# Performance work log

Measured on AMD Instinct MI355X. Metric: run time of the kernel, lower is better.

The kernel has to match this reference:

```python
import jax, jax.numpy as jnp
import numpy as np

N_NODES, N_EDGES, D_FEAT, HIDDEN, N_CLASSES = 100000, 3200000, 128, 16, 40


def setup_inputs() -> dict:
    key = jax.random.key(0)
    ks = jax.random.split(key, 6)
    x = jax.random.normal(ks[0], (N_NODES, D_FEAT), dtype=jnp.float32)
    edge_index = jax.random.randint(ks[1], (2, N_EDGES), 0, N_NODES, dtype=jnp.int32)
    # SAGEConv params: lin_l (aggregated neighbors, with bias), lin_r (root, no bias)
    W_l = jax.random.normal(ks[2], (D_FEAT, HIDDEN), dtype=jnp.float32) / np.sqrt(D_FEAT)
    b_l = jnp.zeros((HIDDEN,), jnp.float32)
    W_r = jax.random.normal(ks[3], (D_FEAT, HIDDEN), dtype=jnp.float32) / np.sqrt(D_FEAT)
    # final Linear(hidden, num_classes)
    W3 = jax.random.normal(ks[4], (HIDDEN, N_CLASSES), dtype=jnp.float32) / np.sqrt(HIDDEN)
    b3 = jnp.zeros((N_CLASSES,), jnp.float32)
    return {"x": x, "edge_index": edge_index, "W_l": W_l, "b_l": b_l,
            "W_r": W_r, "W3": W3, "b3": b3}


def reference(x, edge_index, W_l, b_l, W_r, W3, b3):
    N = x.shape[0]
    src, dst = edge_index[0], edge_index[1]
    # mean aggregation of source features onto target nodes (PyG source_to_target)
    agg = jax.ops.segment_sum(x[src], dst, num_segments=N)            # [N, F]
    deg = jax.ops.segment_sum(jnp.ones_like(dst, dtype=x.dtype), dst, num_segments=N)
    mean = agg / jnp.maximum(deg, 1.0)[:, None]                        # zero-in-degree -> 0
    # SAGEConv: lin_l(mean) + lin_r(x)
    h = mean @ W_l + b_l + x @ W_r                                     # [N, 16]
    h = jax.nn.relu(h)
    logits = h @ W3 + b3                                               # [N, C]
    return jax.nn.log_softmax(logits, axis=1)
```

## Files before the change

kernel.cpp:

```cpp
#include <hip/hip_runtime.h>
#include <hip/hip_bf16.h>

#define D_FEAT 128
#define HIDDEN 16
#define NCLS 40
#define EPB 4096
#define FXSCALE 262144.0f
#define FXINV   (1.0f / 262144.0f)

typedef unsigned int uint;

__device__ __forceinline__ uint f2bf(float x) {
  uint u = __float_as_uint(x);
  return (u + 0x7FFFu + ((u >> 16) & 1u)) >> 16;
}

__global__ __launch_bounds__(256) void lin_kernel(
    const float* __restrict__ x,
    const float* __restrict__ Wl, const float* __restrict__ Wr,
    uint* __restrict__ ylb, float* __restrict__ yr, int N) {
  __shared__ float sW[D_FEAT][8][4];
  __shared__ float sx[32][132];

  int tid = threadIdx.x;
  for (int idx = tid; idx < D_FEAT * 32; idx += 256) {
    int k = idx >> 5, o = idx & 31;
    float v = (o < 16) ? Wl[k * 16 + o] : Wr[k * 16 + (o - 16)];
    sW[k][o >> 2][o & 3] = v;
  }

  int row0 = blockIdx.x * 32;
  for (int q = tid; q < 32 * 32; q += 256) {
    int r = q >> 5, k4 = q & 31;
    int row = row0 + r;
    float4 v = make_float4(0.f, 0.f, 0.f, 0.f);
    if (row < N) v = *(const float4*)(x + (size_t)row * D_FEAT + k4 * 4);
    *(float4*)(&sx[r][k4 * 4]) = v;
  }
  __syncthreads();

  int r = tid >> 3, oq = tid & 7;
  int row = row0 + r;
  if (row < N) {
    float4 acc = make_float4(0.f, 0.f, 0.f, 0.f);
#pragma unroll
    for (int k = 0; k < D_FEAT; ++k) {
      float xv = sx[r][k];
      const float4 w = *(const float4*)(&sW[k][oq][0]);
      acc.x += xv * w.x; acc.y += xv * w.y;
      acc.z += xv * w.z; acc.w += xv * w.w;
    }
    if (oq < 4) {
      uint2 pk;
      pk.x = f2bf(acc.x) | (f2bf(acc.y) << 16);
      pk.y = f2bf(acc.z) | (f2bf(acc.w) << 16);
      *(uint2*)(ylb + (size_t)row * 8 + oq * 2) = pk;
    } else {
      *(float4*)(yr + (size_t)row * 16 + (oq - 4) * 4) = acc;
    }
  }
}

__global__ __launch_bounds__(256) void pass1_kernel(
    const int* __restrict__ src, const int* __restrict__ dst,
    int* __restrict__ gcur1, int* __restrict__ buf1,
    int E, int C, int R1) {
  __shared__ int lh[32], loff[32], gbase[32];
  __shared__ int lbuf[EPB];
  __shared__ int ldst[EPB];
  int tid = threadIdx.x;
  if (tid < 32) lh[tid] = 0;
  __syncthreads();

  int base = blockIdx.x * EPB;
  int key[16], rnk[16], rec[16];
#pragma unroll
  for (int j = 0; j < 16; ++j) {
    int e = base + j * 256 + tid;
    bool ok = e < E;
    int d = ok ? dst[e] : 0;
    int s = ok ? src[e] : 0;
    key[j] = ok ? (d >> 12) : -1;
    rec[j] = s | ((d & 4095) << 17);
    if (ok) rnk[j] = atomicAdd(&lh[key[j]], 1);
  }
  __syncthreads();

  if (tid < 64) {
    int v = (tid < 32) ? lh[tid] : 0;
    int inc = v;
#pragma unroll
    for (int dd = 1; dd < 32; dd <<= 1) {
      int t = __shfl_up(inc, dd);
      if ((int)tid >= dd) inc += t;
    }
    if (tid < 32) {
      loff[tid] = inc - v;
      gbase[tid] = (v && tid < C) ? atomicAdd(&gcur1[tid], v) : 0;
    }
  }
  __syncthreads();

#pragma unroll
  for (int j = 0; j < 16; ++j) {
    if (key[j] >= 0) {
      int p = loff[key[j]] + rnk[j];
      lbuf[p] = rec[j];
      int gp = gbase[key[j]] + rnk[j];
      ldst[p] = (gp < R1) ? key[j] * R1 + gp : -1;
    }
  }
  __syncthreads();

  int tot = min(EPB, E - base);
  for (int i = tid; i < tot; i += 256) {
    int di = ldst[i];
    if (di >= 0) buf1[di] = lbuf[i];
  }
}

__global__ __launch_bounds__(256) void pass2_kernel(
    const int* __restrict__ buf1, const int* __restrict__ gcur1,
    int* __restrict__ gcur, int* __restrict__ packed,
    int C, int R1, int RF, int chunks) {
  int c = blockIdx.x / chunks;
  int chunk = blockIdx.x - c * chunks;
  int cnt1 = min(gcur1[c], R1);
  int base = chunk * EPB;
  int tot = cnt1 - base;
  if (tot <= 0) return;
  tot = min(tot, EPB);

  __shared__ int lh[32], loff[32], gbase[32];
  __shared__ int lbuf[EPB];
  __shared__ int ldst[EPB];
  int tid = threadIdx.x;
  if (tid < 32) lh[tid] = 0;
  __syncthreads();

  const int* in = buf1 + (size_t)c * R1 + base;
  int key[16], rnk[16], rec[16];
#pragma unroll
  for (int j = 0; j < 16; ++j) {
    int i = j * 256 + tid;
    bool ok = i < tot;
    int r = ok ? in[i] : 0;
    int d12 = (r >> 17) & 4095;
    key[j] = ok ? (d12 >> 7) : -1;
    rec[j] = (r & 0x1FFFF) | ((d12 & 127) << 20);
    if (ok) rnk[j] = atomicAdd(&lh[key[j]], 1);
  }
  __syncthreads();

  if (tid < 64) {
    int v = (tid < 32) ? lh[tid] : 0;
    int inc = v;
#pragma unroll
    for (int dd = 1; dd < 32; dd <<= 1) {
      int t = __shfl_up(inc, dd);
      if ((int)tid >= dd) inc += t;
    }
    if (tid < 32) {
      loff[tid] = inc - v;
      gbase[tid] = v ? atomicAdd(&gcur[c * 32 + tid], v) : 0;
    }
  }
  __syncthreads();

#pragma unroll
  for (int j = 0; j < 16; ++j) {
    if (key[j] >= 0) {
      int p = loff[key[j]] + rnk[j];
      lbuf[p] = rec[j];
      int gp = gbase[key[j]] + rnk[j];
      ldst[p] = (gp < RF) ? (c * 32 + key[j]) * RF + gp : -1;
    }
  }
  __syncthreads();

  for (int i = tid; i < tot; i += 256) {
    int di = ldst[i];
    if (di >= 0) packed[di] = lbuf[i];
  }
}

#define ADDI2(ip, idx, u) do {                                              \
    float _lo = __uint_as_float((u) << 16);                                  \
    float _hi = __uint_as_float((u) & 0xFFFF0000u);                          \
    atomicAdd((ip) + (idx),     __float2int_rn(_lo * FXSCALE));              \
    atomicAdd((ip) + (idx) + 1, __float2int_rn(_hi * FXSCALE));              \
  } while (0)

__global__ __launch_bounds__(1024) void baggr_kernel(
    const uint* __restrict__ ylb, const int* __restrict__ packed,
    const int* __restrict__ gcur, float* __restrict__ agg,
    int* __restrict__ count, int N, int RF) {
  __shared__ int sagg[128 * 17];
  __shared__ int sdeg[128];
  int tid = threadIdx.x;
  int b = blockIdx.x;
  for (int i = tid; i < 128 * 17; i += 1024) sagg[i] = 0;
  if (tid < 128) sdeg[tid] = 0;
  __syncthreads();

  int cnt = min(gcur[b], RF);
  int lo = b * RF, hi = lo + cnt;
  for (int e = lo + tid; e < hi; e += 2048) {
    int eb = e + 1024;
    bool has2 = eb < hi;
    int p0 = packed[e];
    int p1 = packed[has2 ? eb : e];
    int s0 = p0 & 0xFFFFF, d0 = (p0 >> 20) & 127;
    int s1 = p1 & 0xFFFFF, d1 = (p1 >> 20) & 127;
    const uint4* q0 = (const uint4*)(ylb + (size_t)s0 * 8);
    const uint4* q1 = (const uint4*)(ylb + (size_t)s1 * 8);
    uint4 a0 = q0[0], a1 = q0[1];
    uint4 b0 = q1[0], b1 = q1[1];

    int* ip0 = &sagg[d0 * 17];
    ADDI2(ip0, 0,  a0.x); ADDI2(ip0, 2,  a0.y);
    ADDI2(ip0, 4,  a0.z); ADDI2(ip0, 6,  a0.w);
    ADDI2(ip0, 8,  a1.x); ADDI2(ip0, 10, a1.y);
    ADDI2(ip0, 12, a1.z); ADDI2(ip0, 14, a1.w);
    atomicAdd(&sdeg[d0], 1);
    if (has2) {
      int* ip1 = &sagg[d1 * 17];
      ADDI2(ip1, 0,  b0.x); ADDI2(ip1, 2,  b0.y);
      ADDI2(ip1, 4,  b0.z); ADDI2(ip1, 6,  b0.w);
      ADDI2(ip1, 8,  b1.x); ADDI2(ip1, 10, b1.y);
      ADDI2(ip1, 12, b1.z); ADDI2(ip1, 14, b1.w);
      atomicAdd(&sdeg[d1], 1);
    }
  }
  __syncthreads();

  int node0 = b * 128;
  for (int i = tid; i < 128 * 16; i += 1024) {
    int node = node0 + (i >> 4);
    if (node < N)
      agg[(size_t)node0 * 16 + i] =
          (float)sagg[(i >> 4) * 17 + (i & 15)] * FXINV;
  }
  if (tid < 128 && node0 + tid < N) count[node0 + tid] = sdeg[tid];
}

__global__ __launch_bounds__(256) void finish_kernel(
    const float* __restrict__ agg, const int* __restrict__ count,
    const float* __restrict__ yr, const float* __restrict__ bl,
    const float* __restrict__ W3, const float* __restrict__ b3,
    float* __restrict__ out, int N) {
  __shared__ float sW3[16 * NCLS];
  __shared__ float sb3[NCLS];
  __shared__ float sbl[16];
  __shared__ float slog[256][NCLS + 1];

  int tid = threadIdx.x;
  for (int idx = tid; idx < 16 * NCLS; idx += 256) sW3[idx] = W3[idx];
  if (tid < NCLS) sb3[tid] = b3[tid];
  if (tid < 16) sbl[tid] = bl[tid];
  __syncthreads();

  int row0 = blockIdx.x * 256;
  int n = row0 + tid;
  if (n < N) {
    float inv = 1.0f / fmaxf((float)count[n], 1.0f);
    float h[16];
#pragma unroll
    for (int k = 0; k < 16; ++k)
      h[k] = fmaxf(agg[(size_t)n * 16 + k] * inv + sbl[k] + yr[(size_t)n * 16 + k], 0.0f);

    float lg[NCLS];
#pragma unroll
    for (int c = 0; c < NCLS; ++c) lg[c] = sb3[c];
#pragma unroll
    for (int k = 0; k < 16; ++k) {
      float hv = h[k];
#pragma unroll
      for (int c = 0; c < NCLS; ++c) lg[c] += hv * sW3[k * NCLS + c];
    }

    float m = lg[0];
#pragma unroll
    for (int c = 1; c < NCLS; ++c) m = fmaxf(m, lg[c]);
    float ssum = 0.f;
#pragma unroll
    for (int c = 0; c < NCLS; ++c) ssum += __expf(lg[c] - m);
    float lse = m + __logf(ssum);
#pragma unroll
    for (int c = 0; c < NCLS; ++c) slog[tid][c] = lg[c] - lse;
  }
  __syncthreads();

  int cnt = min(256, N - row0);
  int total = cnt * NCLS;
  for (int idx = tid; idx < total; idx += 256) {
    int r = idx / NCLS, c = idx - r * NCLS;
    out[(size_t)row0 * NCLS + idx] = slog[r][c];
  }
}

extern "C" void kernel_launch(void* const* d_in, const int* in_sizes, int n_in,
                              void* d_out, int out_size, void* d_ws, size_t ws_size,
                              hipStream_t stream) {
  const float* x   = (const float*)d_in[0];
  const int* eidx  = (const int*)d_in[1];
  const float* Wl  = (const float*)d_in[2];
  const float* bl  = (const float*)d_in[3];
  const float* Wr  = (const float*)d_in[4];
  const float* W3  = (const float*)d_in[5];
  const float* b3  = (const float*)d_in[6];
  float* out = (float*)d_out;

  int N = in_sizes[0] / D_FEAT;
  int E = in_sizes[1] / 2;
  const int* src = eidx;
  const int* dst = eidx + E;

  int C = (N + 4095) >> 12;
  int chunks = (E / C) / EPB + 2;
  int R1 = chunks * EPB;
  int Bf = C * 32;
  int B = (N + 127) >> 7;
  long long m = (long long)E * 128 / N;
  int RF = (int)((m + m / 8 + 511) / 512 * 512);

  size_t n16 = (size_t)N * 16;
  uint* ylb   = (uint*)d_ws;
  int* gcur   = (int*)(ylb + (size_t)N * 8);
  int* gcur1  = gcur + Bf;
  int* packed = gcur1 + C;
  int* buf1   = packed + (size_t)Bf * RF;
  float* agg  = (float*)buf1;
  int* count  = (int*)(agg + n16);
  float* yr   = (float*)(count + N);

  hipMemsetAsync(gcur, 0, (size_t)(Bf + C) * sizeof(int), stream);

  int nb1 = (E + EPB - 1) / EPB;
  pass1_kernel<<<nb1, 256, 0, stream>>>(src, dst, gcur1, buf1, E, C, R1);

  pass2_kernel<<<C * chunks, 256, 0, stream>>>(buf1, gcur1, gcur, packed,
                                               C, R1, RF, chunks);

  lin_kernel<<<(N + 31) / 32, 256, 0, stream>>>(x, Wl, Wr, ylb, yr, N);

  baggr_kernel<<<B, 1024, 0, stream>>>(ylb, packed, gcur, agg, count, N, RF);

  finish_kernel<<<(N + 255) / 256, 256, 0, stream>>>(agg, count, yr, bl, W3, b3, out, N);
}
```

Measured before the change: 110.4 us.

## Fuse finish epilogue into bucketed aggregation kernel, drop agg/count round trip

Merges the separate finish kernel into the block aggregation kernel, so each block computes the ReLU, the 16x40 projection and log_softmax straight from its shared-memory sums and degrees. Each node is handled by 8 threads that each own 5 classes and combine max and sum with xor shuffles. This removes the global write and read of agg and count and one kernel launch. The workspace layout is rearranged so yr no longer overlaps buf1 and packed no longer overlaps buf1. The epilogue adds shared-memory use and a second barrier to the 1024-thread aggregation blocks.

Measured after the change: 108.8 us. About the same (-1.4%).

```diff
diff --git a/kernel.cpp b/kernel.cpp
--- a/kernel.cpp
+++ b/kernel.cpp
@@ -191,16 +191,30 @@
     atomicAdd((ip) + (idx) + 1, __float2int_rn(_hi * FXSCALE));              \
   } while (0)
 
-__global__ __launch_bounds__(1024) void baggr_kernel(
+__global__ __launch_bounds__(1024) void baggrf_kernel(
     const uint* __restrict__ ylb, const int* __restrict__ packed,
-    const int* __restrict__ gcur, float* __restrict__ agg,
-    int* __restrict__ count, int N, int RF) {
+    const int* __restrict__ gcur, const float* __restrict__ yr,
+    const float* __restrict__ bl, const float* __restrict__ W3,
+    const float* __restrict__ b3, float* __restrict__ out,
+    int N, int RF) {
   __shared__ int sagg[128 * 17];
   __shared__ int sdeg[128];
+  __shared__ float syr[128 * 16];
+  __shared__ float sW3[16 * NCLS];
+  __shared__ float sb3[NCLS];
+  __shared__ float sbl[16];
   int tid = threadIdx.x;
   int b = blockIdx.x;
+  int node0 = b * 128;
+
   for (int i = tid; i < 128 * 17; i += 1024) sagg[i] = 0;
   if (tid < 128) sdeg[tid] = 0;
+  if (tid >= 1024 - 640 && tid < 1024 - 640 + 640) {
+    int i = tid - (1024 - 640);
+    sW3[i] = W3[i];
+  }
+  if (tid < NCLS) sb3[tid] = b3[tid];
+  if (tid >= 64 && tid < 80) sbl[tid - 64] = bl[tid - 64];
   __syncthreads();
 
   int cnt = min(gcur[b], RF);
@@ -232,70 +246,48 @@
       atomicAdd(&sdeg[d1], 1);
     }
   }
-  __syncthreads();
-
-  int node0 = b * 128;
-  for (int i = tid; i < 128 * 16; i += 1024) {
-    int node = node0 + (i >> 4);
-    if (node < N)
-      agg[(size_t)node0 * 16 + i] =
-          (float)sagg[(i >> 4) * 17 + (i & 15)] * FXINV;
-  }
-  if (tid < 128 && node0 + tid < N) count[node0 + tid] = sdeg[tid];
-}
-
-__global__ __launch_bounds__(256) void finish_kernel(
-    const float* __restrict__ agg, const int* __restrict__ count,
-    const float* __restrict__ yr, const float* __restrict__ bl,
-    const float* __restrict__ W3, const float* __restrict__ b3,
-    float* __restrict__ out, int N) {
-  __shared__ float sW3[16 * NCLS];
-  __shared__ float sb3[NCLS];
-  __shared__ float sbl[16];
-  __shared__ float slog[256][NCLS + 1];
-
-  int tid = threadIdx.x;
-  for (int idx = tid; idx < 16 * NCLS; idx += 256) sW3[idx] = W3[idx];
-  if (tid < NCLS) sb3[tid] = b3[tid];
-  if (tid < 16) sbl[tid] = bl[tid];
-  __syncthreads();
-
-  int row0 = blockIdx.x * 256;
-  int n = row0 + tid;
+
+  int nvalid = min(128, N - node0);
+  if (nvalid > 0) {
+    int tot16 = nvalid * 16;
+    for (int i = tid; i < tot16; i += 1024)
+      syr[i] = yr[(size_t)node0 * 16 + i];
+  }
+  __syncthreads();
+
+  int node = tid >> 3, q = tid & 7;
+  int n = node0 + node;
   if (n < N) {
-    float inv = 1.0f / fmaxf((float)count[n], 1.0f);
+    float inv = 1.0f / fmaxf((float)sdeg[node], 1.0f);
     float h[16];
 #pragma unroll
     for (int k = 0; k < 16; ++k)
-      h[k] = fmaxf(agg[(size_t)n * 16 + k] * inv + sbl[k] + yr[(size_t)n * 16 + k], 0.0f);
-
-    float lg[NCLS];
-#pragma unroll
-    for (int c = 0; c < NCLS; ++c) lg[c] = sb3[c];
+      h[k] = fmaxf((float)sagg[node * 17 + k] * (FXINV) * inv + sbl[k] +
+                       syr[node * 16 + k],
+                   0.0f);
+    float lg[5];
+#pragma unroll
+    for (int j = 0; j < 5; ++j) lg[j] = sb3[q * 5 + j];
 #pragma unroll
     for (int k = 0; k < 16; ++k) {
       float hv = h[k];
 #pragma unroll
-      for (int c = 0; c < NCLS; ++c) lg[c] += hv * sW3[k * NCLS + c];
-    }
-
+      for (int j = 0; j < 5; ++j) lg[j] += hv * sW3[k * NCLS + q * 5 + j];
+    }
     float m = lg[0];
 #pragma unroll
-    for (int c = 1; c < NCLS; ++c) m = fmaxf(m, lg[c]);
-    float ssum = 0.f;
-#pragma unroll
-    for (int c = 0; c < NCLS; ++c) ssum += __expf(lg[c] - m);
-    float lse = m + __logf(ssum);
-#pragma unroll
-    for (int c = 0; c < NCLS; ++c) slog[tid][c] = lg[c] - lse;
-  }
-  __syncthreads();
-
-  int cnt = min(256, N - row0);
-  int total = cnt * NCLS;
-  for (int idx = tid; idx < total; idx += 256) {
-    int r = idx / NCLS, c = idx - r * NCLS;
-    out[(size_t)row0 * NCLS + idx] = slog[r][c];
+    for (int j = 1; j < 5; ++j) m = fmaxf(m, lg[j]);
+#pragma unroll
+    for (int dd = 1; dd < 8; dd <<= 1) m = fmaxf(m, __shfl_xor(m, dd));
+    float s = 0.f;
+#pragma unroll
+    for (int j = 0; j < 5; ++j) s += __expf(lg[j] - m);
+#pragma unroll
+    for (int dd = 1; dd < 8; dd <<= 1) s += __shfl_xor(s, dd);
+    float lse = m + __logf(s);
+    float* op = out + (size_t)n * NCLS + q * 5;
+#pragma unroll
+    for (int j = 0; j < 5; ++j) op[j] = lg[j] - lse;
   }
 }
 
@@ -326,13 +318,11 @@
 
   size_t n16 = (size_t)N * 16;
   uint* ylb   = (uint*)d_ws;
-  int* gcur   = (int*)(ylb + (size_t)N * 8);
+  float* yr   = (float*)(ylb + (size_t)N * 8);
+  int* gcur   = (int*)(yr + n16);
   int* gcur1  = gcur + Bf;
-  int* packed = gcur1 + C;
-  int* buf1   = packed + (size_t)Bf * RF;
-  float* agg  = (float*)buf1;
-  int* count  = (int*)(agg + n16);
-  float* yr   = (float*)(count + N);
+  int* buf1   = gcur1 + C;
+  int* packed = buf1 + (size_t)C * R1;
 
   hipMemsetAsync(gcur, 0, (size_t)(Bf + C) * sizeof(int), stream);
 
@@ -344,7 +334,6 @@
 
   lin_kernel<<<(N + 31) / 32, 256, 0, stream>>>(x, Wl, Wr, ylb, yr, N);
 
-  baggr_kernel<<<B, 1024, 0, stream>>>(ylb, packed, gcur, agg, count, N, RF);
-
-  finish_kernel<<<(N + 255) / 256, 256, 0, stream>>>(agg, count, yr, bl, W3, b3, out, N);
-}
+  baggrf_kernel<<<B, 1024, 0, stream>>>(ylb, packed, gcur, yr, bl, W3, b3,
+                                        out, N, RF);
+}
```
